# Kernel tuning notes

Hardware: AMD Instinct MI355X
Metric: run time of the kernel (lower is better)

Reference implementation:

```python
import jax, jax.numpy as jnp
import numpy as np

H = 12          # num_attention_heads
D = 64          # attention_head_size
HID = H * D     # hidden_size = 768
M = 1024        # max_position_embeddings


def setup_inputs() -> dict:
    key = jax.random.key(0)
    ks = jax.random.split(key, 9)
    B, S = 4, 1024
    s = 0.02
    return {
        "hidden_states": jax.random.normal(ks[0], (B, S, HID), jnp.float32),
        "attention_mask": jnp.zeros((B, 1, 1, S), jnp.float32),
        "Wq": jax.random.normal(ks[1], (HID, HID), jnp.float32) * s,
        "bq": jnp.zeros((HID,), jnp.float32),
        "Wk": jax.random.normal(ks[2], (HID, HID), jnp.float32) * s,
        "bk": jnp.zeros((HID,), jnp.float32),
        "Wv": jax.random.normal(ks[3], (HID, HID), jnp.float32) * s,
        "bv": jnp.zeros((HID,), jnp.float32),
        "dist_emb": jax.random.normal(ks[4], (2 * M - 1, D), jnp.float32) * s,
    }


def reference(hidden_states, attention_mask, Wq, bq, Wk, bk, Wv, bv, dist_emb):
    B, S, _ = hidden_states.shape

    def heads(x):  # [B,S,HID] -> [B,H,S,D]
        return x.reshape(B, S, H, D).transpose(0, 2, 1, 3)

    q = heads(hidden_states @ Wq + bq)
    k = heads(hidden_states @ Wk + bk)
    v = heads(hidden_states @ Wv + bv)

    # raw dot-product scores [B,H,S,S]
    scores = jnp.einsum('bhld,bhrd->bhlr', q, k)

    # relative_key_query positional bias
    pos = jnp.arange(S)
    distance = pos[:, None] - pos[None, :] + (M - 1)   # [S,S] in [0, 2M-2]
    pe = dist_emb[distance]                            # [S,S,D]
    scores = scores + jnp.einsum('bhld,lrd->bhlr', q, pe) \
                    + jnp.einsum('bhrd,lrd->bhlr', k, pe)

    scores = scores / jnp.sqrt(jnp.asarray(D, scores.dtype)) + attention_mask
    probs = jax.nn.softmax(scores, axis=-1)            # dropout is identity in eval

    ctx = jnp.einsum('bhlr,bhrd->bhld', probs, v)      # [B,H,S,D]
    ctx = ctx.transpose(0, 2, 1, 3).reshape(B, S, HID)
    return ctx, probs
```

## Files before the change

kernel.cpp:

```cpp
#include <hip/hip_runtime.h>
#include <hip/hip_bf16.h>

#define DEVFN __device__ __forceinline__

typedef __bf16 bf16x8 __attribute__((ext_vector_type(8)));
typedef float f32x4 __attribute__((ext_vector_type(4)));
typedef unsigned short ushort8 __attribute__((ext_vector_type(8)));
typedef unsigned short us4 __attribute__((ext_vector_type(4)));

namespace {

constexpr int S = 1024;
constexpr int HID = 768;
constexpr int NH = 12;
constexpr int HD = 64;

DEVFN unsigned short f2bf(float f) {
  union { float f; unsigned u; } v; v.f = f;
  unsigned r = v.u + 0x7FFF + ((v.u >> 16) & 1);
  return (unsigned short)(r >> 16);
}

DEVFN float bf2f(unsigned short u) {
  union { unsigned u; float f; } v; v.u = ((unsigned)u) << 16; return v.f;
}

DEVFN f32x4 zero4() { return f32x4{0.f, 0.f, 0.f, 0.f}; }

DEVFN f32x4 mfma_bf16(bf16x8 a, bf16x8 b, f32x4 c) {
  return __builtin_amdgcn_mfma_f32_16x16x32_bf16(a, b, c, 0, 0, 0);
}

DEVFN void gload16(void* lds_base, const void* gsrc) {
  __builtin_amdgcn_global_load_lds(
      (const __attribute__((address_space(1))) void*)gsrc,
      (__attribute__((address_space(3))) void*)lds_base, 16, 0, 0);
}

DEVFN bf16x8 frag_ld(const char* tile, int row, int ch) {
  int chs = ch ^ (row & 7);
  return *(const bf16x8*)(tile + row * 128 + chs * 16);
}

__global__ void k0_cvt_x(const float* __restrict__ x, unsigned short* __restrict__ xb) {
  size_t i = (size_t)(blockIdx.x * 256 + threadIdx.x) * 8;
  float4 a = *(const float4*)(x + i);
  float4 c = *(const float4*)(x + i + 4);
  ushort8 o;
  o[0] = f2bf(a.x); o[1] = f2bf(a.y); o[2] = f2bf(a.z); o[3] = f2bf(a.w);
  o[4] = f2bf(c.x); o[5] = f2bf(c.y); o[6] = f2bf(c.z); o[7] = f2bf(c.w);
  *(ushort8*)(xb + i) = o;
}

__global__ void k0_cvt_pe(const float* __restrict__ de, unsigned short* __restrict__ peb) {
  size_t i = (size_t)(blockIdx.x * 256 + threadIdx.x) * 8;
  int row = (int)(i >> 6);
  ushort8 o;
  if (row < 2047) {
    float4 a = *(const float4*)(de + i);
    float4 c = *(const float4*)(de + i + 4);
    o[0] = f2bf(a.x); o[1] = f2bf(a.y); o[2] = f2bf(a.z); o[3] = f2bf(a.w);
    o[4] = f2bf(c.x); o[5] = f2bf(c.y); o[6] = f2bf(c.z); o[7] = f2bf(c.w);
  } else {
    o = ushort8{0, 0, 0, 0, 0, 0, 0, 0};
  }
  *(ushort8*)(peb + i) = o;
}

__global__ __launch_bounds__(256) void k0_wt(const float* __restrict__ Wq,
                                             const float* __restrict__ Wk,
                                             const float* __restrict__ Wv,
                                             unsigned short* __restrict__ wt) {
  __shared__ float t[64][65];
  int bidx = blockIdx.x;
  int sec = bidx / 144, rem = bidx % 144;
  int ktb = rem / 12, ntb = rem % 12;
  const float* W = (sec == 0) ? Wq : ((sec == 1) ? Wk : Wv);
  int k0 = ktb * 64, n0 = ntb * 64;
  int tid = threadIdx.x;
  #pragma unroll
  for (int p = 0; p < 4; ++p) {
    int id = p * 256 + tid;
    int row = id >> 4, ch = id & 15;
    float4 v = *(const float4*)(W + (size_t)(k0 + row) * 768 + n0 + ch * 4);
    t[row][ch * 4 + 0] = v.x; t[row][ch * 4 + 1] = v.y;
    t[row][ch * 4 + 2] = v.z; t[row][ch * 4 + 3] = v.w;
  }
  __syncthreads();
  #pragma unroll
  for (int p = 0; p < 2; ++p) {
    int id = p * 256 + tid;
    int nrow = id >> 3, c8 = id & 7;
    ushort8 o;
    #pragma unroll
    for (int i = 0; i < 8; ++i) o[i] = f2bf(t[c8 * 8 + i][nrow]);
    *(ushort8*)(wt + (size_t)(sec * 768 + n0 + nrow) * 768 + k0 + c8 * 8) = o;
  }
}

__global__ __launch_bounds__(256) void k1_qkv(
    const unsigned short* __restrict__ xb, const unsigned short* __restrict__ wt,
    const float* __restrict__ bq, const float* __restrict__ bk, const float* __restrict__ bv,
    unsigned short* __restrict__ q_ws, unsigned short* __restrict__ k_ws,
    unsigned short* __restrict__ vt_ws) {
  __shared__ char ldsA[8192], ldsB[8192];
  const int tid = threadIdx.x, lane = tid & 63, wv = tid >> 6;
  const int row16 = lane & 15, cgrp = lane >> 4;
  const int ntb = blockIdx.x % 36, mtb = blockIdx.x / 36;
  const int sec = ntb / 12;
  const int n0 = ntb * 64;
  const int m0 = mtb * 64;

  f32x4 acc[4] = {zero4(), zero4(), zero4(), zero4()};

  for (int k0 = 0; k0 < 768; k0 += 64) {
    #pragma unroll
    for (int c = 0; c < 2; ++c) {
      int cc = (wv * 2 + c) * 64 + lane;
      int row = cc >> 3, ch = cc & 7, chs = ch ^ (row & 7);
      gload16(ldsA + (wv * 2 + c) * 1024, xb + (size_t)(m0 + row) * 768 + k0 + chs * 8);
      gload16(ldsB + (wv * 2 + c) * 1024, wt + (size_t)(n0 + row) * 768 + k0 + chs * 8);
    }
    __syncthreads();
    if (sec < 2) {
      bf16x8 af[2];
      #pragma unroll
      for (int k2 = 0; k2 < 2; ++k2) af[k2] = frag_ld(ldsA, wv * 16 + row16, k2 * 4 + cgrp);
      #pragma unroll
      for (int nt = 0; nt < 4; ++nt)
        #pragma unroll
        for (int k2 = 0; k2 < 2; ++k2) {
          bf16x8 bf = frag_ld(ldsB, nt * 16 + row16, k2 * 4 + cgrp);
          acc[nt] = mfma_bf16(af[k2], bf, acc[nt]);
        }
    } else {
      bf16x8 af[2];
      #pragma unroll
      for (int k2 = 0; k2 < 2; ++k2) af[k2] = frag_ld(ldsB, wv * 16 + row16, k2 * 4 + cgrp);
      #pragma unroll
      for (int mt = 0; mt < 4; ++mt)
        #pragma unroll
        for (int k2 = 0; k2 < 2; ++k2) {
          bf16x8 bx = frag_ld(ldsA, mt * 16 + row16, k2 * 4 + cgrp);
          acc[mt] = mfma_bf16(af[k2], bx, acc[mt]);
        }
    }
    __syncthreads();
  }

  if (sec < 2) {
    unsigned short* dst = (sec == 0) ? q_ws : k_ws;
    const float* bias = (sec == 0) ? bq : bk;
    int nl0 = (ntb % 12) * 64;
    #pragma unroll
    for (int nt = 0; nt < 4; ++nt) {
      int nn = nl0 + nt * 16 + row16;
      float bb = bias[nn];
      int hh = nn >> 6, dd = nn & 63;
      #pragma unroll
      for (int j = 0; j < 4; ++j) {
        int m = m0 + wv * 16 + cgrp * 4 + j;
        int b_ = m >> 10, s_ = m & 1023;
        dst[(size_t)((b_ * 12 + hh) * 1024 + s_) * 64 + dd] = f2bf(acc[nt][j] + bb);
      }
    }
  } else {
    int nl0 = (ntb % 12) * 64;
    #pragma unroll
    for (int j = 0; j < 4; ++j) {
      int nn = nl0 + wv * 16 + cgrp * 4 + j;
      float bb = bv[nn];
      int hh = nn >> 6, dd = nn & 63;
      #pragma unroll
      for (int mt = 0; mt < 4; ++mt) {
        int m = m0 + mt * 16 + row16;
        int b_ = m >> 10, s_ = m & 1023;
        vt_ws[(size_t)((b_ * 12 + hh) * 64 + dd) * 1024 + s_] = f2bf(acc[mt][j] + bb);
      }
    }
  }
}

template <int PF32>
__global__ __launch_bounds__(256) void k2_score(
    const unsigned short* __restrict__ q_ws, const unsigned short* __restrict__ k_ws,
    const unsigned short* __restrict__ peb, const float* __restrict__ mask,
    void* __restrict__ p_out, float* __restrict__ rsum_part) {
  __shared__ char k_lds[8192];
  __shared__ char pe_lds[16384];
  __shared__ unsigned short s3t[4][64 * 36];
  __shared__ unsigned short p_sh[64 * 64];
  __shared__ float rsum_sh[2][64];

  const int tid = threadIdx.x, lane = tid & 63, wv = tid >> 6;
  const int wl = wv >> 1, wr = wv & 1;
  const int row16 = lane & 15, cgrp = lane >> 4;

  const int bid = blockIdx.x;
  const int rt = bid & 15, lt = (bid >> 4) & 15, bh = bid >> 8;
  const int b = bh / NH;
  const int l0 = lt * 64, r0 = rt * 64;

  const unsigned short* qh = q_ws + (size_t)bh * S * HD;
  const unsigned short* khp = k_ws + (size_t)bh * S * HD;
  const float* maskb = mask + b * S;

  #pragma unroll
  for (int c = 0; c < 2; ++c) {
    int cc = (wv * 2 + c) * 64 + lane;
    int row = cc >> 3, ch = cc & 7, chs = ch ^ (row & 7);
    gload16(k_lds + (wv * 2 + c) * 1024, khp + (size_t)(r0 + row) * HD + chs * 8);
  }
  {
    int m0 = l0 - r0 + 960;
    #pragma unroll
    for (int c = 0; c < 4; ++c) {
      int cc = (wv * 4 + c) * 64 + lane;
      int row = cc >> 3, ch = cc & 7, chs = ch ^ (row & 7);
      gload16(pe_lds + (wv * 4 + c) * 1024, peb + (size_t)(m0 + row) * HD + chs * 8);
    }
  }

  bf16x8 qf[2][2];
  #pragma unroll
  for (int ltl = 0; ltl < 2; ++ltl)
    #pragma unroll
    for (int k2 = 0; k2 < 2; ++k2)
      qf[ltl][k2] = *(const bf16x8*)(qh + (size_t)(l0 + wl * 32 + ltl * 16 + row16) * HD +
                                     k2 * 32 + cgrp * 8);
  __syncthreads();

  bf16x8 kf[2][2], pef[4][2];
  #pragma unroll
  for (int rtl = 0; rtl < 2; ++rtl)
    #pragma unroll
    for (int k2 = 0; k2 < 2; ++k2)
      kf[rtl][k2] = frag_ld(k_lds, wr * 32 + rtl * 16 + row16, k2 * 4 + cgrp);
  const int qb = (wl - wr) * 32 + 32;
  #pragma unroll
  for (int jt = 0; jt < 4; ++jt)
    #pragma unroll
    for (int k2 = 0; k2 < 2; ++k2)
      pef[jt][k2] = frag_ld(pe_lds, qb + jt * 16 + row16, k2 * 4 + cgrp);

  unsigned short* s3w = &s3t[wv][0];

  #pragma unroll
  for (int rtl = 0; rtl < 2; ++rtl)
    #pragma unroll
    for (int jt = 0; jt < 4; ++jt) {
      f32x4 a3 = zero4();
      a3 = mfma_bf16(kf[rtl][0], pef[jt][0], a3);
      a3 = mfma_bf16(kf[rtl][1], pef[jt][1], a3);
      us4 o;
      o[0] = f2bf(a3[0]); o[1] = f2bf(a3[1]); o[2] = f2bf(a3[2]); o[3] = f2bf(a3[3]);
      *(us4*)(s3w + (jt * 16 + row16) * 36 + rtl * 16 + cgrp * 4) = o;
    }

  f32x4 s1[2][2];
  #pragma unroll
  for (int ltl = 0; ltl < 2; ++ltl)
    #pragma unroll
    for (int rtl = 0; rtl < 2; ++rtl) {
      f32x4 a1 = zero4();
      a1 = mfma_bf16(qf[ltl][0], kf[rtl][0], a1);
      a1 = mfma_bf16(qf[ltl][1], kf[rtl][1], a1);
      s1[ltl][rtl] = a1;
    }
  f32x4 s2[2][4];
  #pragma unroll
  for (int ltl = 0; ltl < 2; ++ltl)
    #pragma unroll
    for (int jt = 0; jt < 4; ++jt) {
      f32x4 a2 = zero4();
      a2 = mfma_bf16(qf[ltl][0], pef[jt][0], a2);
      a2 = mfma_bf16(qf[ltl][1], pef[jt][1], a2);
      s2[ltl][jt] = a2;
    }

  float rs[2][4] = {};
  #pragma unroll
  for (int rtl = 0; rtl < 2; ++rtl) {
    float mval = maskb[r0 + wr * 32 + rtl * 16 + row16];
    #pragma unroll
    for (int ltl = 0; ltl < 2; ++ltl) {
      const int jtA = ltl - rtl + 1;
      #pragma unroll
      for (int j = 0; j < 4; ++j) {
        int dl = ltl * 16 + cgrp * 4 + j;
        int dr = rtl * 16 + row16;
        int jjq = dl - dr + 31;
        int src = (lane & 48) | (jjq & 15);
        float vA = __shfl(s2[ltl][jtA][j], src, 64);
        float vB = __shfl(s2[ltl][jtA + 1][j], src, 64);
        float b1 = ((jjq >> 4) == jtA) ? vA : vB;
        float b2 = bf2f(s3w[jjq * 36 + dr]);
        float logit = (s1[ltl][rtl][j] + b1 + b2) * 0.125f + mval;
        float p = __expf(logit);
        rs[ltl][j] += p;
        int dlb = wl * 32 + dl, drb = wr * 32 + dr;
        p_sh[dlb * 64 + (drb ^ ((dlb & 7) << 3))] = f2bf(p);
      }
    }
  }

  #pragma unroll
  for (int ltl = 0; ltl < 2; ++ltl)
    #pragma unroll
    for (int j = 0; j < 4; ++j) {
      float v = rs[ltl][j];
      v += __shfl_xor(v, 1, 64);
      v += __shfl_xor(v, 2, 64);
      v += __shfl_xor(v, 4, 64);
      v += __shfl_xor(v, 8, 64);
      rs[ltl][j] = v;
    }
  if (row16 == 0) {
    #pragma unroll
    for (int ltl = 0; ltl < 2; ++ltl)
      #pragma unroll
      for (int j = 0; j < 4; ++j)
        rsum_sh[wr][wl * 32 + ltl * 16 + cgrp * 4 + j] = rs[ltl][j];
  }
  __syncthreads();

  if (tid < 64)
    rsum_part[((size_t)(bh * 16 + lt) * 64 + tid) * 16 + rt] =
        rsum_sh[0][tid] + rsum_sh[1][tid];

  #pragma unroll
  for (int p2 = 0; p2 < 2; ++p2) {
    int id = p2 * 256 + tid, dl = id >> 3, c = id & 7;
    uint4 w = *(const uint4*)((const char*)p_sh + dl * 128 + (c ^ (dl & 7)) * 16);
    if (PF32 == 0) {
      *(uint4*)((unsigned short*)p_out + ((size_t)bh * S + l0 + dl) * S + r0 + c * 8) = w;
    } else {
      const unsigned short* pu = (const unsigned short*)&w;
      float* dst = (float*)p_out + ((size_t)bh * S + l0 + dl) * S + r0 + c * 8;
      float4 lo{bf2f(pu[0]), bf2f(pu[1]), bf2f(pu[2]), bf2f(pu[3])};
      float4 hi{bf2f(pu[4]), bf2f(pu[5]), bf2f(pu[6]), bf2f(pu[7])};
      *(float4*)dst = lo; *(float4*)(dst + 4) = hi;
    }
  }
}

template <int PF32>
__global__ __launch_bounds__(256) void k3_pv(
    const void* __restrict__ p_in, const unsigned short* __restrict__ vt_ws,
    const float* __restrict__ rsum_part, float* __restrict__ out_ctx,
    float* __restrict__ out_probs) {
  constexpr int TB = PF32 ? 16384 : 8192;
  __shared__ char p_sh[2][TB];
  __shared__ float inv_sh[64];

  const int tid = threadIdx.x, lane = tid & 63, wv = tid >> 6;
  const int row16 = lane & 15, cgrp = lane >> 4;
  const int bid = blockIdx.x;
  const int lt = bid & 15, bh = bid >> 4;
  const int b = bh / NH, h = bh % NH;
  const int l0 = lt * 64;

  const unsigned short* vth = vt_ws + (size_t)bh * HD * S;
  float* probs_bh = out_probs + (size_t)bh * S * S;

  if (tid < 64) {
    const float4* pp =
        (const float4*)(rsum_part + ((size_t)(bh * 16 + lt) * 64 + tid) * 16);
    float s = 0.f;
    #pragma unroll
    for (int i = 0; i < 4; ++i) {
      float4 v = pp[i];
      s += v.x + v.y + v.z + v.w;
    }
    inv_sh[tid] = 1.0f / s;
  }

  auto stage = [&](char* buf, int r0) {
    if (PF32 == 0) {
      #pragma unroll
      for (int c = 0; c < 2; ++c) {
        int cc = (wv * 2 + c) * 64 + lane;
        int row = cc >> 3, ch = cc & 7, chs = ch ^ (row & 7);
        gload16(buf + (wv * 2 + c) * 1024,
                (const unsigned short*)p_in + ((size_t)bh * S + l0 + row) * S + r0 + chs * 8);
      }
    } else {
      #pragma unroll
      for (int c = 0; c < 4; ++c) {
        int cc = (wv * 4 + c) * 64 + lane;
        int row = cc >> 4, ch = cc & 15, chs = ch ^ (row & 15);
        gload16(buf + (wv * 4 + c) * 1024,
                (const float*)p_in + ((size_t)bh * S + l0 + row) * S + r0 + chs * 4);
      }
    }
  };

  stage(p_sh[0], 0);
  __syncthreads();

  f32x4 ctxacc[4] = {zero4(), zero4(), zero4(), zero4()};

  for (int rt = 0; rt < 16; ++rt) {
    const int r0 = rt * 64, cur = rt & 1;
    if (rt < 15) stage(p_sh[cur ^ 1], r0 + 64);
    const char* cb = p_sh[cur];

    if (PF32 == 0) {
      #pragma unroll
      for (int p2 = 0; p2 < 2; ++p2) {
        int id = p2 * 256 + tid, dl = id >> 3, c = id & 7;
        uint4 w = *(const uint4*)(cb + dl * 128 + (c ^ (dl & 7)) * 16);
        const unsigned short* pu = (const unsigned short*)&w;
        float iv = inv_sh[dl];
        float* dst = probs_bh + (size_t)(l0 + dl) * S + r0 + c * 8;
        float4 lo{bf2f(pu[0]) * iv, bf2f(pu[1]) * iv, bf2f(pu[2]) * iv, bf2f(pu[3]) * iv};
        float4 hi{bf2f(pu[4]) * iv, bf2f(pu[5]) * iv, bf2f(pu[6]) * iv, bf2f(pu[7]) * iv};
        *(float4*)dst = lo; *(float4*)(dst + 4) = hi;
      }
    } else {
      #pragma unroll
      for (int p2 = 0; p2 < 4; ++p2) {
        int id = p2 * 256 + tid, dl = id >> 4, c = id & 15;
        float4 v = *(const float4*)(cb + dl * 256 + ((c ^ (dl & 15)) * 16));
        float iv = inv_sh[dl];
        v.x *= iv; v.y *= iv; v.z *= iv; v.w *= iv;
        *(float4*)(probs_bh + (size_t)(l0 + dl) * S + r0 + c * 4) = v;
      }
    }

    {
      int lrow = wv * 16 + row16;
      bf16x8 pa[2];
      if (PF32 == 0) {
        #pragma unroll
        for (int kc = 0; kc < 2; ++kc) {
          int ch = kc * 4 + cgrp, chs = ch ^ (lrow & 7);
          pa[kc] = *(const bf16x8*)(cb + lrow * 128 + chs * 16);
        }
      } else {
        #pragma unroll
        for (int kc = 0; kc < 2; ++kc) {
          int c0 = kc * 8 + cgrp * 2;
          float4 f0 = *(const float4*)(cb + lrow * 256 + ((c0 ^ (lrow & 15)) * 16));
          float4 f1 = *(const float4*)(cb + lrow * 256 + (((c0 + 1) ^ (lrow & 15)) * 16));
          union { ushort8 u; bf16x8 bv; } cv;
          const float* ff0 = (const float*)&f0;
          const float* ff1 = (const float*)&f1;
          #pragma unroll
          for (int i = 0; i < 4; ++i) {
            union { float f; unsigned u; } t0; t0.f = ff0[i];
            union { float f; unsigned u; } t1; t1.f = ff1[i];
            cv.u[i] = (unsigned short)(t0.u >> 16);
            cv.u[i + 4] = (unsigned short)(t1.u >> 16);
          }
          pa[kc] = cv.bv;
        }
      }
      #pragma unroll
      for (int dt = 0; dt < 4; ++dt) {
        bf16x8 vb0 = *(const bf16x8*)(vth + (size_t)(dt * 16 + row16) * S + r0 + cgrp * 8);
        bf16x8 vb1 = *(const bf16x8*)(vth + (size_t)(dt * 16 + row16) * S + r0 + 32 + cgrp * 8);
        ctxacc[dt] = mfma_bf16(pa[0], vb0, ctxacc[dt]);
        ctxacc[dt] = mfma_bf16(pa[1], vb1, ctxacc[dt]);
      }
    }
    __syncthreads();
  }

  #pragma unroll
  for (int dt = 0; dt < 4; ++dt)
    #pragma unroll
    for (int j = 0; j < 4; ++j) {
      int lr = wv * 16 + cgrp * 4 + j;
      out_ctx[((size_t)(b * S + l0 + lr)) * HID + h * HD + dt * 16 + row16] =
          ctxacc[dt][j] * inv_sh[lr];
    }
}

}

extern "C" void kernel_launch(void* const* d_in, const int* in_sizes, int n_in,
                              void* d_out, int out_size, void* d_ws, size_t ws_size,
                              hipStream_t stream) {
  const float* hidden = (const float*)d_in[0];
  const float* mask   = (const float*)d_in[1];
  const float* Wq = (const float*)d_in[2];
  const float* bq = (const float*)d_in[3];
  const float* Wk = (const float*)d_in[4];
  const float* bk = (const float*)d_in[5];
  const float* Wv = (const float*)d_in[6];
  const float* bv = (const float*)d_in[7];
  const float* de = (const float*)d_in[8];

  unsigned short* ws = (unsigned short*)d_ws;
  unsigned short* q_ws  = ws;
  unsigned short* k_ws  = ws + 3145728;
  unsigned short* vt_ws = ws + 6291456;
  unsigned short* xb    = ws + 9437184;
  unsigned short* wt    = ws + 12582912;
  unsigned short* peb   = ws + 14352384;
  float* rsum_part = (float*)(ws + 14483456);
  unsigned short* p_ws  = ws + 14483456 + 1572864;

  const size_t need_big = ((size_t)14483456 + 1572864 + 50331648) * 2;
  const bool big = ws_size >= need_big;

  float* outc = (float*)d_out;
  float* outp = outc + (size_t)4 * 1024 * 768;

  hipLaunchKernelGGL(k0_cvt_x, dim3(1536), dim3(256), 0, stream, hidden, xb);
  hipLaunchKernelGGL(k0_cvt_pe, dim3(64), dim3(256), 0, stream, de, peb);
  hipLaunchKernelGGL(k0_wt, dim3(432), dim3(256), 0, stream, Wq, Wk, Wv, wt);
  hipLaunchKernelGGL(k1_qkv, dim3(2304), dim3(256), 0, stream,
                     xb, wt, bq, bk, bv, q_ws, k_ws, vt_ws);
  if (big) {
    k2_score<0><<<dim3(12288), dim3(256), 0, stream>>>(q_ws, k_ws, peb, mask,
                                                       (void*)p_ws, rsum_part);
    k3_pv<0><<<dim3(768), dim3(256), 0, stream>>>((const void*)p_ws, vt_ws, rsum_part,
                                                  outc, outp);
  } else {
    k2_score<1><<<dim3(12288), dim3(256), 0, stream>>>(q_ws, k_ws, peb, mask,
                                                       (void*)outp, rsum_part);
    k3_pv<1><<<dim3(768), dim3(256), 0, stream>>>((const void*)outp, vt_ws, rsum_part,
                                                  outc, outp);
  }
}
```

Measured before the change: 208.4 us.

## Enlarge QKV GEMM tiles and split PV over key quarters with reduction kernel

The QKV projection kernel now uses 128x128 tiles with a 2x2 wave layout and a 4x4 accumulator grid per wave instead of 64x64 tiles, raising data reuse per LDS load. The PV kernel is split into four key-range quarters per row tile, giving 3072 blocks instead of 768 for better occupancy. Partial context sums go to a workspace and a new reduction kernel adds and normalises them. The fp32 fallback path for small workspaces is removed, so the code now assumes a large workspace, and the partial buffers add extra memory traffic.

```diff
diff --git a/kernel.cpp b/kernel.cpp
--- a/kernel.cpp
+++ b/kernel.cpp
@@ -103,89 +103,108 @@
     const float* __restrict__ bq, const float* __restrict__ bk, const float* __restrict__ bv,
     unsigned short* __restrict__ q_ws, unsigned short* __restrict__ k_ws,
     unsigned short* __restrict__ vt_ws) {
-  __shared__ char ldsA[8192], ldsB[8192];
+  __shared__ char ldsA[16384], ldsB[16384];
   const int tid = threadIdx.x, lane = tid & 63, wv = tid >> 6;
   const int row16 = lane & 15, cgrp = lane >> 4;
-  const int ntb = blockIdx.x % 36, mtb = blockIdx.x / 36;
-  const int sec = ntb / 12;
-  const int n0 = ntb * 64;
-  const int m0 = mtb * 64;
-
-  f32x4 acc[4] = {zero4(), zero4(), zero4(), zero4()};
+  const int wm = wv >> 1, wn = wv & 1;
+  const int ntb = blockIdx.x % 18, mtb = blockIdx.x / 18;
+  const int sec = ntb / 6;
+  const int n0 = ntb * 128;
+  const int m0 = mtb * 128;
+
+  f32x4 acc[4][4];
+  #pragma unroll
+  for (int i = 0; i < 4; ++i)
+    #pragma unroll
+    for (int j = 0; j < 4; ++j) acc[i][j] = zero4();
 
   for (int k0 = 0; k0 < 768; k0 += 64) {
     #pragma unroll
-    for (int c = 0; c < 2; ++c) {
-      int cc = (wv * 2 + c) * 64 + lane;
+    for (int c = 0; c < 4; ++c) {
+      int cc = (wv * 4 + c) * 64 + lane;
       int row = cc >> 3, ch = cc & 7, chs = ch ^ (row & 7);
-      gload16(ldsA + (wv * 2 + c) * 1024, xb + (size_t)(m0 + row) * 768 + k0 + chs * 8);
-      gload16(ldsB + (wv * 2 + c) * 1024, wt + (size_t)(n0 + row) * 768 + k0 + chs * 8);
+      gload16(ldsA + (wv * 4 + c) * 1024, xb + (size_t)(m0 + row) * 768 + k0 + chs * 8);
+      gload16(ldsB + (wv * 4 + c) * 1024, wt + (size_t)(n0 + row) * 768 + k0 + chs * 8);
     }
     __syncthreads();
     if (sec < 2) {
-      bf16x8 af[2];
-      #pragma unroll
-      for (int k2 = 0; k2 < 2; ++k2) af[k2] = frag_ld(ldsA, wv * 16 + row16, k2 * 4 + cgrp);
+      bf16x8 bf[4][2];
       #pragma unroll
       for (int nt = 0; nt < 4; ++nt)
         #pragma unroll
-        for (int k2 = 0; k2 < 2; ++k2) {
-          bf16x8 bf = frag_ld(ldsB, nt * 16 + row16, k2 * 4 + cgrp);
-          acc[nt] = mfma_bf16(af[k2], bf, acc[nt]);
+        for (int k2 = 0; k2 < 2; ++k2)
+          bf[nt][k2] = frag_ld(ldsB, wn * 64 + nt * 16 + row16, k2 * 4 + cgrp);
+      #pragma unroll
+      for (int mt = 0; mt < 4; ++mt) {
+        bf16x8 af0 = frag_ld(ldsA, wm * 64 + mt * 16 + row16, cgrp);
+        bf16x8 af1 = frag_ld(ldsA, wm * 64 + mt * 16 + row16, 4 + cgrp);
+        #pragma unroll
+        for (int nt = 0; nt < 4; ++nt) {
+          acc[mt][nt] = mfma_bf16(af0, bf[nt][0], acc[mt][nt]);
+          acc[mt][nt] = mfma_bf16(af1, bf[nt][1], acc[mt][nt]);
         }
+      }
     } else {
-      bf16x8 af[2];
-      #pragma unroll
-      for (int k2 = 0; k2 < 2; ++k2) af[k2] = frag_ld(ldsB, wv * 16 + row16, k2 * 4 + cgrp);
+      bf16x8 am[4][2];
       #pragma unroll
       for (int mt = 0; mt < 4; ++mt)
         #pragma unroll
-        for (int k2 = 0; k2 < 2; ++k2) {
-          bf16x8 bx = frag_ld(ldsA, mt * 16 + row16, k2 * 4 + cgrp);
-          acc[mt] = mfma_bf16(af[k2], bx, acc[mt]);
+        for (int k2 = 0; k2 < 2; ++k2)
+          am[mt][k2] = frag_ld(ldsA, wm * 64 + mt * 16 + row16, k2 * 4 + cgrp);
+      #pragma unroll
+      for (int nt = 0; nt < 4; ++nt) {
+        bf16x8 bv0 = frag_ld(ldsB, wn * 64 + nt * 16 + row16, cgrp);
+        bf16x8 bv1 = frag_ld(ldsB, wn * 64 + nt * 16 + row16, 4 + cgrp);
+        #pragma unroll
+        for (int mt = 0; mt < 4; ++mt) {
+          acc[nt][mt] = mfma_bf16(bv0, am[mt][0], acc[nt][mt]);
+          acc[nt][mt] = mfma_bf16(bv1, am[mt][1], acc[nt][mt]);
         }
+      }
     }
     __syncthreads();
   }
 
+  const int nl0 = (ntb % 6) * 128;
   if (sec < 2) {
     unsigned short* dst = (sec == 0) ? q_ws : k_ws;
     const float* bias = (sec == 0) ? bq : bk;
-    int nl0 = (ntb % 12) * 64;
     #pragma unroll
     for (int nt = 0; nt < 4; ++nt) {
-      int nn = nl0 + nt * 16 + row16;
+      int nn = nl0 + wn * 64 + nt * 16 + row16;
       float bb = bias[nn];
       int hh = nn >> 6, dd = nn & 63;
       #pragma unroll
+      for (int mt = 0; mt < 4; ++mt)
+        #pragma unroll
+        for (int j = 0; j < 4; ++j) {
+          int m = m0 + wm * 64 + mt * 16 + cgrp * 4 + j;
+          int b_ = m >> 10, s_ = m & 1023;
+          dst[(size_t)((b_ * 12 + hh) * 1024 + s_) * 64 + dd] = f2bf(acc[mt][nt][j] + bb);
+        }
+    }
+  } else {
+    #pragma unroll
+    for (int nt = 0; nt < 4; ++nt)
+      #pragma unroll
       for (int j = 0; j < 4; ++j) {
-        int m = m0 + wv * 16 + cgrp * 4 + j;
-        int b_ = m >> 10, s_ = m & 1023;
-        dst[(size_t)((b_ * 12 + hh) * 1024 + s_) * 64 + dd] = f2bf(acc[nt][j] + bb);
+        int nn = nl0 + wn * 64 + nt * 16 + cgrp * 4 + j;
+        float bb = bv[nn];
+        int hh = nn >> 6, dd = nn & 63;
+        #pragma unroll
+        for (int mt = 0; mt < 4; ++mt) {
+          int m = m0 + wm * 64 + mt * 16 + row16;
+          int b_ = m >> 10, s_ = m & 1023;
+          vt_ws[(size_t)((b_ * 12 + hh) * 64 + dd) * 1024 + s_] = f2bf(acc[nt][mt][j] + bb);
+        }
       }
-    }
-  } else {
-    int nl0 = (ntb % 12) * 64;
-    #pragma unroll
-    for (int j = 0; j < 4; ++j) {
-      int nn = nl0 + wv * 16 + cgrp * 4 + j;
-      float bb = bv[nn];
-      int hh = nn >> 6, dd = nn & 63;
-      #pragma unroll
-      for (int mt = 0; mt < 4; ++mt) {
-        int m = m0 + mt * 16 + row16;
-        int b_ = m >> 10, s_ = m & 1023;
-        vt_ws[(size_t)((b_ * 12 + hh) * 64 + dd) * 1024 + s_] = f2bf(acc[mt][j] + bb);
-      }
-    }
-  }
-}
-
-template <int PF32>
+  }
+}
+
 __global__ __launch_bounds__(256) void k2_score(
     const unsigned short* __restrict__ q_ws, const unsigned short* __restrict__ k_ws,
     const unsigned short* __restrict__ peb, const float* __restrict__ mask,
-    void* __restrict__ p_out, float* __restrict__ rsum_part) {
+    unsigned short* __restrict__ p_out, float* __restrict__ rsum_part) {
   __shared__ char k_lds[8192];
   __shared__ char pe_lds[16384];
   __shared__ unsigned short s3t[4][64 * 36];
@@ -332,33 +351,21 @@
   for (int p2 = 0; p2 < 2; ++p2) {
     int id = p2 * 256 + tid, dl = id >> 3, c = id & 7;
     uint4 w = *(const uint4*)((const char*)p_sh + dl * 128 + (c ^ (dl & 7)) * 16);
-    if (PF32 == 0) {
-      *(uint4*)((unsigned short*)p_out + ((size_t)bh * S + l0 + dl) * S + r0 + c * 8) = w;
-    } else {
-      const unsigned short* pu = (const unsigned short*)&w;
-      float* dst = (float*)p_out + ((size_t)bh * S + l0 + dl) * S + r0 + c * 8;
-      float4 lo{bf2f(pu[0]), bf2f(pu[1]), bf2f(pu[2]), bf2f(pu[3])};
-      float4 hi{bf2f(pu[4]), bf2f(pu[5]), bf2f(pu[6]), bf2f(pu[7])};
-      *(float4*)dst = lo; *(float4*)(dst + 4) = hi;
-    }
-  }
-}
-
-template <int PF32>
+    *(uint4*)(p_out + ((size_t)bh * S + l0 + dl) * S + r0 + c * 8) = w;
+  }
+}
+
 __global__ __launch_bounds__(256) void k3_pv(
-    const void* __restrict__ p_in, const unsigned short* __restrict__ vt_ws,
-    const float* __restrict__ rsum_part, float* __restrict__ out_ctx,
-    float* __restrict__ out_probs) {
-  constexpr int TB = PF32 ? 16384 : 8192;
-  __shared__ char p_sh[2][TB];
+    const unsigned short* __restrict__ p_in, const unsigned short* __restrict__ vt_ws,
+    const float* __restrict__ rsum_part, float* __restrict__ ctx_part,
+    float* __restrict__ inv_ws, float* __restrict__ out_probs) {
+  __shared__ char p_sh[2][8192];
   __shared__ float inv_sh[64];
 
   const int tid = threadIdx.x, lane = tid & 63, wv = tid >> 6;
   const int row16 = lane & 15, cgrp = lane >> 4;
-  const int bid = blockIdx.x;
-  const int lt = bid & 15, bh = bid >> 4;
-  const int b = bh / NH, h = bh % NH;
-  const int l0 = lt * 64;
+  const int rq = blockIdx.x & 3, lt = (blockIdx.x >> 2) & 15, bh = blockIdx.x >> 6;
+  const int l0 = lt * 64, rbase = rq * 256;
 
   const unsigned short* vth = vt_ws + (size_t)bh * HD * S;
   float* probs_bh = out_probs + (size_t)bh * S * S;
@@ -372,89 +379,50 @@
       float4 v = pp[i];
       s += v.x + v.y + v.z + v.w;
     }
-    inv_sh[tid] = 1.0f / s;
+    float iv = 1.0f / s;
+    inv_sh[tid] = iv;
+    if (rq == 0) inv_ws[bh * S + l0 + tid] = iv;
   }
 
   auto stage = [&](char* buf, int r0) {
-    if (PF32 == 0) {
-      #pragma unroll
-      for (int c = 0; c < 2; ++c) {
-        int cc = (wv * 2 + c) * 64 + lane;
-        int row = cc >> 3, ch = cc & 7, chs = ch ^ (row & 7);
-        gload16(buf + (wv * 2 + c) * 1024,
-                (const unsigned short*)p_in + ((size_t)bh * S + l0 + row) * S + r0 + chs * 8);
-      }
-    } else {
-      #pragma unroll
-      for (int c = 0; c < 4; ++c) {
-        int cc = (wv * 4 + c) * 64 + lane;
-        int row = cc >> 4, ch = cc & 15, chs = ch ^ (row & 15);
-        gload16(buf + (wv * 4 + c) * 1024,
-                (const float*)p_in + ((size_t)bh * S + l0 + row) * S + r0 + chs * 4);
-      }
+    #pragma unroll
+    for (int c = 0; c < 2; ++c) {
+      int cc = (wv * 2 + c) * 64 + lane;
+      int row = cc >> 3, ch = cc & 7, chs = ch ^ (row & 7);
+      gload16(buf + (wv * 2 + c) * 1024,
+              p_in + ((size_t)bh * S + l0 + row) * S + r0 + chs * 8);
     }
   };
 
-  stage(p_sh[0], 0);
+  stage(p_sh[0], rbase);
   __syncthreads();
 
   f32x4 ctxacc[4] = {zero4(), zero4(), zero4(), zero4()};
 
-  for (int rt = 0; rt < 16; ++rt) {
-    const int r0 = rt * 64, cur = rt & 1;
-    if (rt < 15) stage(p_sh[cur ^ 1], r0 + 64);
+  for (int it = 0; it < 4; ++it) {
+    const int r0 = rbase + it * 64, cur = it & 1;
+    if (it < 3) stage(p_sh[cur ^ 1], r0 + 64);
     const char* cb = p_sh[cur];
 
-    if (PF32 == 0) {
-      #pragma unroll
-      for (int p2 = 0; p2 < 2; ++p2) {
-        int id = p2 * 256 + tid, dl = id >> 3, c = id & 7;
-        uint4 w = *(const uint4*)(cb + dl * 128 + (c ^ (dl & 7)) * 16);
-        const unsigned short* pu = (const unsigned short*)&w;
-        float iv = inv_sh[dl];
-        float* dst = probs_bh + (size_t)(l0 + dl) * S + r0 + c * 8;
-        float4 lo{bf2f(pu[0]) * iv, bf2f(pu[1]) * iv, bf2f(pu[2]) * iv, bf2f(pu[3]) * iv};
-        float4 hi{bf2f(pu[4]) * iv, bf2f(pu[5]) * iv, bf2f(pu[6]) * iv, bf2f(pu[7]) * iv};
-        *(float4*)dst = lo; *(float4*)(dst + 4) = hi;
-      }
-    } else {
-      #pragma unroll
-      for (int p2 = 0; p2 < 4; ++p2) {
-        int id = p2 * 256 + tid, dl = id >> 4, c = id & 15;
-        float4 v = *(const float4*)(cb + dl * 256 + ((c ^ (dl & 15)) * 16));
-        float iv = inv_sh[dl];
-        v.x *= iv; v.y *= iv; v.z *= iv; v.w *= iv;
-        *(float4*)(probs_bh + (size_t)(l0 + dl) * S + r0 + c * 4) = v;
-      }
+    #pragma unroll
+    for (int p2 = 0; p2 < 2; ++p2) {
+      int id = p2 * 256 + tid, dl = id >> 3, c = id & 7;
+      uint4 w = *(const uint4*)(cb + dl * 128 + (c ^ (dl & 7)) * 16);
+      const unsigned short* pu = (const unsigned short*)&w;
+      float iv = inv_sh[dl];
+      float* dst = probs_bh + (size_t)(l0 + dl) * S + r0 + c * 8;
+      float4 lo{bf2f(pu[0]) * iv, bf2f(pu[1]) * iv, bf2f(pu[2]) * iv, bf2f(pu[3]) * iv};
+      float4 hi{bf2f(pu[4]) * iv, bf2f(pu[5]) * iv, bf2f(pu[6]) * iv, bf2f(pu[7]) * iv};
+      *(float4*)dst = lo; *(float4*)(dst + 4) = hi;
     }
 
     {
       int lrow = wv * 16 + row16;
       bf16x8 pa[2];
-      if (PF32 == 0) {
-        #pragma unroll
-        for (int kc = 0; kc < 2; ++kc) {
-          int ch = kc * 4 + cgrp, chs = ch ^ (lrow & 7);
-          pa[kc] = *(const bf16x8*)(cb + lrow * 128 + chs * 16);
-        }
-      } else {
-        #pragma unroll
-        for (int kc = 0; kc < 2; ++kc) {
-          int c0 = kc * 8 + cgrp * 2;
-          float4 f0 = *(const float4*)(cb + lrow * 256 + ((c0 ^ (lrow & 15)) * 16));
-          float4 f1 = *(const float4*)(cb + lrow * 256 + (((c0 + 1) ^ (lrow & 15)) * 16));
-          union { ushort8 u; bf16x8 bv; } cv;
-          const float* ff0 = (const float*)&f0;
-          const float* ff1 = (const float*)&f1;
-          #pragma unroll
-          for (int i = 0; i < 4; ++i) {
-            union { float f; unsigned u; } t0; t0.f = ff0[i];
-            union { float f; unsigned u; } t1; t1.f = ff1[i];
-            cv.u[i] = (unsigned short)(t0.u >> 16);
-            cv.u[i + 4] = (unsigned short)(t1.u >> 16);
-          }
-          pa[kc] = cv.bv;
-        }
+      #pragma unroll
+      for (int kc = 0; kc < 2; ++kc) {
+        int ch = kc * 4 + cgrp, chs = ch ^ (lrow & 7);
+        pa[kc] = *(const bf16x8*)(cb + lrow * 128 + chs * 16);
       }
       #pragma unroll
       for (int dt = 0; dt < 4; ++dt) {
@@ -472,9 +440,33 @@
     #pragma unroll
     for (int j = 0; j < 4; ++j) {
       int lr = wv * 16 + cgrp * 4 + j;
-      out_ctx[((size_t)(b * S + l0 + lr)) * HID + h * HD + dt * 16 + row16] =
-          ctxacc[dt][j] * inv_sh[lr];
-    }
+      ctx_part[((size_t)(rq * 48 + bh) * S + l0 + lr) * 64 + dt * 16 + row16] =
+          ctxacc[dt][j];
+    }
+}
+
+__global__ __launch_bounds__(256) void k4_red(
+    const float* __restrict__ ctx_part, const float* __restrict__ inv_ws,
+    float* __restrict__ out_ctx) {
+  int gid = blockIdx.x * 256 + threadIdx.x;
+  int t = gid >> 3, d0 = (gid & 7) * 8;
+  int bh = t >> 10, l = t & 1023;
+  float4 s0{0.f, 0.f, 0.f, 0.f}, s1{0.f, 0.f, 0.f, 0.f};
+  #pragma unroll
+  for (int rq = 0; rq < 4; ++rq) {
+    const float* p = ctx_part + ((size_t)(rq * 48 + bh) * S + l) * 64 + d0;
+    float4 a = *(const float4*)p;
+    float4 b = *(const float4*)(p + 4);
+    s0.x += a.x; s0.y += a.y; s0.z += a.z; s0.w += a.w;
+    s1.x += b.x; s1.y += b.y; s1.z += b.z; s1.w += b.w;
+  }
+  float iv = inv_ws[t];
+  s0.x *= iv; s0.y *= iv; s0.z *= iv; s0.w *= iv;
+  s1.x *= iv; s1.y *= iv; s1.z *= iv; s1.w *= iv;
+  int b_ = bh / NH, h = bh % NH;
+  float* dst = out_ctx + ((size_t)(b_ * S + l)) * HID + h * HD + d0;
+  *(float4*)dst = s0;
+  *(float4*)(dst + 4) = s1;
 }
 
 }
@@ -500,10 +492,9 @@
   unsigned short* wt    = ws + 12582912;
   unsigned short* peb   = ws + 14352384;
   float* rsum_part = (float*)(ws + 14483456);
-  unsigned short* p_ws  = ws + 14483456 + 1572864;
-
-  const size_t need_big = ((size_t)14483456 + 1572864 + 50331648) * 2;
-  const bool big = ws_size >= need_big;
+  unsigned short* p_ws  = ws + 16056320;
+  float* ctx_part = (float*)(ws + 66387968);
+  float* inv_ws   = (float*)(ws + 91553792);
 
   float* outc = (float*)d_out;
   float* outp = outc + (size_t)4 * 1024 * 768;
@@ -511,17 +502,12 @@
   hipLaunchKernelGGL(k0_cvt_x, dim3(1536), dim3(256), 0, stream, hidden, xb);
   hipLaunchKernelGGL(k0_cvt_pe, dim3(64), dim3(256), 0, stream, de, peb);
   hipLaunchKernelGGL(k0_wt, dim3(432), dim3(256), 0, stream, Wq, Wk, Wv, wt);
-  hipLaunchKernelGGL(k1_qkv, dim3(2304), dim3(256), 0, stream,
+  hipLaunchKernelGGL(k1_qkv, dim3(576), dim3(256), 0, stream,
                      xb, wt, bq, bk, bv, q_ws, k_ws, vt_ws);
-  if (big) {
-    k2_score<0><<<dim3(12288), dim3(256), 0, stream>>>(q_ws, k_ws, peb, mask,
-                                                       (void*)p_ws, rsum_part);
-    k3_pv<0><<<dim3(768), dim3(256), 0, stream>>>((const void*)p_ws, vt_ws, rsum_part,
-                                                  outc, outp);
-  } else {
-    k2_score<1><<<dim3(12288), dim3(256), 0, stream>>>(q_ws, k_ws, peb, mask,
-                                                       (void*)outp, rsum_part);
-    k3_pv<1><<<dim3(768), dim3(256), 0, stream>>>((const void*)outp, vt_ws, rsum_part,
-                                                  outc, outp);
-  }
-}
+  hipLaunchKernelGGL(k2_score, dim3(12288), dim3(256), 0, stream,
+                     q_ws, k_ws, peb, mask, p_ws, rsum_part);
+  hipLaunchKernelGGL(k3_pv, dim3(3072), dim3(256), 0, stream,
+                     p_ws, vt_ws, rsum_part, ctx_part, inv_ws, outp);
+  hipLaunchKernelGGL(k4_red, dim3(1536), dim3(256), 0, stream,
+                     ctx_part, inv_ws, outc);
+}
```

Result: slower. 238.7 us (+14.5%).
